# Performance work log

Measured on AMD Instinct MI355X. Metric: run time of the kernel, lower is better.

Reference implementation:

```python
import jax, jax.numpy as jnp
import numpy as np

N_HEAD = 16
ROPE_BASE = 10000.0


def _rope(x):
    # x: (B, T, H, D), interleaved even/odd (GPT-NeoX style)
    B, T, H, D = x.shape
    inv_freq = 1.0 / (ROPE_BASE ** (jnp.arange(0, D, 2, dtype=jnp.float32) / D))
    t = jnp.arange(T, dtype=jnp.float32)
    freqs = t[:, None] * inv_freq[None, :]            # (T, D//2)
    cos = jnp.cos(freqs)[None, :, None, :]            # (1, T, 1, D//2)
    sin = jnp.sin(freqs)[None, :, None, :]
    x1, x2 = x[..., ::2], x[..., 1::2]
    y1 = x1 * cos - x2 * sin
    y2 = x1 * sin + x2 * cos
    return jnp.stack((y1, y2), axis=-1).reshape(B, T, H, D)


def setup_inputs() -> dict:
    key = jax.random.key(0)
    k1, k2, k3 = jax.random.split(key, 3)
    B, T, C = 4, 2048, 1024
    x = jax.random.normal(k1, (B, T, C), dtype=jnp.float32)
    W_attn = jax.random.normal(k2, (C, 3 * C), dtype=jnp.float32) * (1.0 / np.sqrt(C))
    W_proj = jax.random.normal(k3, (C, C), dtype=jnp.float32) * (1.0 / np.sqrt(C))
    return {"x": x, "W_attn": W_attn, "W_proj": W_proj}


def reference(x, W_attn, W_proj):
    B, T, C = x.shape
    H = N_HEAD
    D = C // H
    qkv = jnp.einsum('btc,cf->btf', x, W_attn)        # (B, T, 3C)
    q, k, v = jnp.split(qkv, 3, axis=-1)
    q = _rope(q.reshape(B, T, H, D))
    k = _rope(k.reshape(B, T, H, D))
    v = v.reshape(B, T, H, D)
    # (B, H, T, D)
    q = q.transpose(0, 2, 1, 3)
    k = k.transpose(0, 2, 1, 3)
    v = v.transpose(0, 2, 1, 3)
    scale = 1.0 / np.sqrt(D).astype(np.float32)
    scores = jnp.einsum('bhqd,bhkd->bhqk', q, k) * scale
    causal = jnp.tril(jnp.ones((T, T), dtype=bool))
    scores = jnp.where(causal[None, None], scores, jnp.finfo(scores.dtype).min)
    att = jax.nn.softmax(scores, axis=-1)
    y = jnp.einsum('bhqk,bhkd->bhqd', att, v)         # (B, H, T, D)
    y = y.transpose(0, 2, 1, 3).reshape(B, T, C)
    return jnp.einsum('btc,cf->btf', y, W_proj)
```

## Files before the change

kernel.cpp:

```cpp
#include <hip/hip_runtime.h>
#include <hip/hip_bf16.h>
#include <math.h>

typedef __attribute__((ext_vector_type(8))) __bf16 bf16x8;
typedef __attribute__((ext_vector_type(4))) float f32x4;
typedef __attribute__((ext_vector_type(16))) float f32x16;
typedef __attribute__((ext_vector_type(4))) unsigned short us4;

#define DEVINL static __device__ __forceinline__

DEVINL unsigned short f2bf(float f) {
  union { float f; unsigned int u; } v; v.f = f;
  return (unsigned short)((v.u + 0x7FFFu + ((v.u >> 16) & 1u)) >> 16);
}

DEVINL unsigned short f2bf_hw(float f) {
  __bf16 h = (__bf16)f;
  union { __bf16 h; unsigned short u; } v; v.h = h;
  return v.u;
}

DEVINL unsigned pk2(float a, float b) {
  return (unsigned)f2bf_hw(a) | ((unsigned)f2bf_hw(b) << 16);
}

DEVINL f32x4 mfma16(bf16x8 a, bf16x8 b, f32x4 c) {
  return __builtin_amdgcn_mfma_f32_16x16x32_bf16(a, b, c, 0, 0, 0);
}
DEVINL f32x16 mfma32(bf16x8 a, bf16x8 b, f32x16 c) {
  return __builtin_amdgcn_mfma_f32_32x32x16_bf16(a, b, c, 0, 0, 0);
}

#define GLOAD16(GP, LP)                                                        \
  __builtin_amdgcn_global_load_lds(                                            \
      (const __attribute__((address_space(1))) void*)(GP),                     \
      (__attribute__((address_space(3))) void*)(LP), 16, 0, 0)

static constexpr int kB = 4, kT = 2048, kC = 1024, kH = 16, kD = 64;
static constexpr int kM = kB * kT;

__global__ __launch_bounds__(256) void prep_kernel(
    const float* __restrict__ x, unsigned short* __restrict__ xb,
    const float* __restrict__ Wa, unsigned short* __restrict__ WaT,
    const float* __restrict__ Wp, unsigned short* __restrict__ WpT,
    float* __restrict__ cosT, float* __restrict__ sinT) {
  const int blk = blockIdx.x;
  if (blk < 2048) {
    const int n4 = kM * kC / 4;
    for (int i = blk * 256 + threadIdx.x; i < n4; i += 2048 * 256) {
      float4 v = ((const float4*)x)[i];
      us4 o;
      o[0] = f2bf(v.x); o[1] = f2bf(v.y); o[2] = f2bf(v.z); o[3] = f2bf(v.w);
      ((us4*)xb)[i] = o;
    }
  } else if (blk < 2048 + 3072 + 1024) {
    __shared__ float tile[32][33];
    int t = blk - 2048;
    const float* W; unsigned short* WT; int N, bx, by;
    if (t < 3072) { W = Wa; WT = WaT; N = 3072; bx = t % 96; by = t / 96; }
    else { t -= 3072; W = Wp; WT = WpT; N = 1024; bx = t % 32; by = t / 32; }
    const int n0 = bx * 32, k0 = by * 32;
    const int tx = threadIdx.x & 31, ty = threadIdx.x >> 5;
#pragma unroll
    for (int i = 0; i < 4; ++i)
      tile[ty + i * 8][tx] = W[(size_t)(k0 + ty + i * 8) * N + n0 + tx];
    __syncthreads();
#pragma unroll
    for (int i = 0; i < 4; ++i)
      WT[(size_t)(n0 + ty + i * 8) * 1024 + k0 + tx] = f2bf(tile[tx][ty + i * 8]);
  } else {
    int idx = (blk - 6144) * 256 + threadIdx.x;
    int d2 = idx >> 11, t = idx & 2047;
    double ang = (double)t * pow(10000.0, -(double)d2 / 32.0);
    cosT[idx] = (float)cos(ang);
    sinT[idx] = (float)sin(ang);
  }
}

template <int EPI>
__global__ __launch_bounds__(512, 2) void gemm_bt_kernel(
    const unsigned short* __restrict__ A, const unsigned short* __restrict__ Bt,
    float* __restrict__ Cout, int Ndim, int Kdim,
    const float* __restrict__ cosT, const float* __restrict__ sinT,
    unsigned short* __restrict__ Qr, unsigned short* __restrict__ Kr,
    unsigned short* __restrict__ Vtg) {
  __shared__ unsigned short As[3][256 * 64];
  __shared__ unsigned short Bs[3][128 * 64];
  const int tid = threadIdx.x;
  const int wave = tid >> 6, lane = tid & 63;

  const int nwg = gridDim.x * gridDim.y;
  const int lin = blockIdx.y * gridDim.x + blockIdx.x;
  const int wg = (lin & 7) * (nwg >> 3) + (lin >> 3);
  const int n0 = (wg % gridDim.x) * 128, m0 = (wg / gridDim.x) * 256;

  const int wr = wave >> 1, wc = wave & 1;

  f32x4 acc[4][4] = {};

  const int fr = lane & 15;
  const int sblk = tid;
  const int srow3 = sblk >> 3, skb = sblk & 7;
  const int sgran = (skb ^ (srow3 & 7)) << 3;

  auto stageA = [&](int t, int l) {
    const int bb = t % 3;
    const int k0 = t << 6;
    const int row = (l << 6) + srow3;
    GLOAD16(A + (size_t)(m0 + row) * Kdim + k0 + sgran,
            &As[bb][(l * 512 + wave * 64) * 8]);
  };
  auto stageB = [&](int t, int l) {
    const int bb = t % 3;
    const int k0 = t << 6;
    const int row = (l << 6) + srow3;
    GLOAD16(Bt + (size_t)(n0 + row) * Kdim + k0 + sgran,
            &Bs[bb][(l * 512 + wave * 64) * 8]);
  };

  const int NT = Kdim >> 6;

  stageA(0, 0); stageA(0, 1); stageA(0, 2); stageA(0, 3);
  stageB(0, 0); stageB(0, 1);
  stageA(1, 0); stageA(1, 1); stageA(1, 2); stageA(1, 3);
  stageB(1, 0); stageB(1, 1);
  asm volatile("s_waitcnt vmcnt(6)" ::: "memory");
  __builtin_amdgcn_sched_barrier(0);
  __builtin_amdgcn_s_barrier();

  const int rx = lane & 7, ku = lane >> 4;

  for (int t = 0; t < NT; ++t) {
    const int buf = t % 3;
    const unsigned char* Ab = (const unsigned char*)As[buf];
    const unsigned char* Bb = (const unsigned char*)Bs[buf];
    bf16x8 af[4], bfr[4];

    {
      const int col = ((ku ^ rx) << 4);
#pragma unroll
      for (int f = 0; f < 4; ++f)
        af[f] = *(const bf16x8*)(Ab + (wr * 64 + f * 16 + fr) * 128 + col);
#pragma unroll
      for (int f = 0; f < 4; ++f)
        bfr[f] = *(const bf16x8*)(Bb + (wc * 64 + f * 16 + fr) * 128 + col);
    }
    if (t + 2 < NT) { stageA(t + 2, 0); stageA(t + 2, 1); stageB(t + 2, 0); }
    __builtin_amdgcn_s_barrier();
    asm volatile("s_waitcnt lgkmcnt(0)" ::: "memory");
    __builtin_amdgcn_sched_barrier(0);
    __builtin_amdgcn_s_setprio(1);
#pragma unroll
    for (int i = 0; i < 4; ++i)
#pragma unroll
      for (int j = 0; j < 4; ++j)
        acc[i][j] = mfma16(af[i], bfr[j], acc[i][j]);
    __builtin_amdgcn_s_setprio(0);
    __builtin_amdgcn_s_barrier();

    {
      const int col = (((4 | ku) ^ rx) << 4);
#pragma unroll
      for (int f = 0; f < 4; ++f)
        af[f] = *(const bf16x8*)(Ab + (wr * 64 + f * 16 + fr) * 128 + col);
#pragma unroll
      for (int f = 0; f < 4; ++f)
        bfr[f] = *(const bf16x8*)(Bb + (wc * 64 + f * 16 + fr) * 128 + col);
    }
    if (t + 2 < NT) { stageA(t + 2, 2); stageA(t + 2, 3); stageB(t + 2, 1); }
    if (t + 2 < NT) {
      asm volatile("s_waitcnt vmcnt(6)" ::: "memory");
    } else if (t + 1 < NT) {
      asm volatile("s_waitcnt vmcnt(0)" ::: "memory");
    }
    __builtin_amdgcn_sched_barrier(0);
    __builtin_amdgcn_s_barrier();
    asm volatile("s_waitcnt lgkmcnt(0)" ::: "memory");
    __builtin_amdgcn_sched_barrier(0);
    __builtin_amdgcn_s_setprio(1);
#pragma unroll
    for (int i = 0; i < 4; ++i)
#pragma unroll
      for (int j = 0; j < 4; ++j)
        acc[i][j] = mfma16(af[i], bfr[j], acc[i][j]);
    __builtin_amdgcn_s_setprio(0);
    __builtin_amdgcn_s_barrier();
  }

  const int lr = (lane >> 4) * 4;
  const int fc = lane & 15;
  if (EPI == 0) {
#pragma unroll
    for (int i = 0; i < 4; ++i) {
      int mb = m0 + wr * 64 + i * 16 + lr;
#pragma unroll
      for (int j = 0; j < 4; ++j) {
        int n = n0 + wc * 64 + j * 16 + fc;
#pragma unroll
        for (int r = 0; r < 4; ++r)
          Cout[(size_t)(mb + r) * Ndim + n] = acc[i][j][r];
      }
    }
  } else {
#pragma unroll
    for (int i = 0; i < 4; ++i) {
      int mb = m0 + wr * 64 + i * 16 + lr;
      int b = mb >> 11, t0 = mb & 2047;
#pragma unroll
      for (int j = 0; j < 4; ++j) {
        int n = n0 + wc * 64 + j * 16 + fc;
        int sec = n >> 10;
        int c = n & 1023;
        int h = c >> 6, d = c & 63;
        size_t bh = (size_t)(b * 16 + h);
        if (sec == 2) {
          us4 pk;
#pragma unroll
          for (int r = 0; r < 4; ++r) pk[r] = f2bf(acc[i][j][r]);
          *(us4*)&Vtg[(bh * 64 + d) * 2048 + t0] = pk;
        } else {
          unsigned short* dst = (sec == 0) ? Qr : Kr;
          float4 c4 = *(const float4*)&cosT[(d >> 1) * 2048 + t0];
          float4 s4 = *(const float4*)&sinT[(d >> 1) * 2048 + t0];
          const float* cp = (const float*)&c4;
          const float* sp = (const float*)&s4;
#pragma unroll
          for (int r = 0; r < 4; ++r) {
            float v = acc[i][j][r];
            float pv = __shfl_xor(v, 1);
            float y = (d & 1) ? fmaf(pv, sp[r], v * cp[r])
                              : fmaf(v, cp[r], -pv * sp[r]);
            dst[(bh * 2048 + t0 + r) * 64 + d] = f2bf(y);
          }
        }
      }
    }
  }
}

__global__ __launch_bounds__(256, 3)
void attn_kernel(const unsigned short* __restrict__ Qr,
                 const unsigned short* __restrict__ Kr,
                 const unsigned short* __restrict__ Vtg,
                 unsigned short* __restrict__ Yb) {
  __shared__ unsigned short Ks[3][64 * 64];
  __shared__ unsigned short Vs[3][64 * 64];

  const int tid = threadIdx.x;
  const int wave = tid >> 6, lane = tid & 63;
  const int q31 = lane & 31, hi = lane >> 5;
  const int srow = lane >> 3;
  const int sblk = (lane & 7) ^ srow;
  const int rswz = (lane & 7) << 4;

  int lin = blockIdx.y * 8 + blockIdx.x;
  int wg = (lin & 7) * 64 + (lin >> 3);
  const int qpair = wg & 7;
  const int bh = wg >> 3;

  const unsigned short* Qg = Qr + (size_t)bh * 2048 * 64;
  const unsigned short* Kg = Kr + (size_t)bh * 2048 * 64;
  const unsigned short* Vg = Vtg + (size_t)bh * 64 * 2048;

  const float c = 0.18033688f;
  const float THR = 44.0f;

  auto stage = [&](int j, int bb) {
    int kv0s = j * 64;
#pragma unroll
    for (int o = 0; o < 2; ++o) {
      int s = o * 4 + wave;
      int row = s * 8 + srow;
      GLOAD16(Kg + ((size_t)(kv0s + row) * 64 + sblk * 8), &Ks[bb][s * 512]);
      GLOAD16(Vg + ((size_t)row * 2048 + kv0s + sblk * 8), &Vs[bb][s * 512]);
    }
  };

  for (int seg = 0; seg < 2; ++seg) {
    const int qblk = seg ? (15 - qpair) : qpair;
    const int qw = qblk * 128 + wave * 32;
    const int qg = qw + q31;
    const int NT = 2 * qblk + 2;

    bf16x8 qf[4];
#pragma unroll
    for (int ds = 0; ds < 4; ++ds)
      qf[ds] = *(const bf16x8*)&Qg[(size_t)qg * 64 + ds * 16 + hi * 8];

    float mrow = -1e30f, lrow = 0.f;
    f32x16 y0 = {}, y1 = {};

    stage(0, 0);
    stage(1, 1);
    asm volatile("s_waitcnt vmcnt(4)" ::: "memory");
    __builtin_amdgcn_sched_barrier(0);
    __builtin_amdgcn_s_barrier();

    for (int t = 0; t < NT; ++t) {
      const int buf = t % 3;
      if (t + 2 < NT) stage(t + 2, (t + 2) % 3);
      __builtin_amdgcn_sched_barrier(0);
      const int kv0 = t * 64;

      if (kv0 <= qw + 31) {
        f32x16 st[2] = {};
        __builtin_amdgcn_s_setprio(1);
#pragma unroll
        for (int sub = 0; sub < 2; ++sub) {
          const unsigned char* kbase =
              (const unsigned char*)Ks[buf] + (sub * 32 + q31) * 128;
#pragma unroll
          for (int ds = 0; ds < 4; ++ds) {
            bf16x8 af = *(const bf16x8*)(kbase + ((ds * 32 + hi * 16) ^ rswz));
            st[sub] = mfma32(af, qf[ds], st[sub]);
          }
        }
        __builtin_amdgcn_s_setprio(0);

        if (kv0 + 63 > qw) {
#pragma unroll
          for (int sub = 0; sub < 2; ++sub)
#pragma unroll
            for (int r = 0; r < 16; ++r) {
              int kv = kv0 + sub * 32 + (r & 3) + 8 * (r >> 2) + 4 * hi;
              if (kv > qg) st[sub][r] = -1e30f;
            }
        }

        float tm = st[0][0];
#pragma unroll
        for (int r = 1; r < 16; ++r) tm = fmaxf(tm, st[0][r]);
#pragma unroll
        for (int r = 0; r < 16; ++r) tm = fmaxf(tm, st[1][r]);
        tm = fmaxf(tm, __shfl_xor(tm, 32));

        if (!__all(tm <= mrow + THR)) {
          float mn = fmaxf(mrow, tm);
          float al = __builtin_amdgcn_exp2f((mrow - mn) * c);
          mrow = mn;
          lrow *= al;
#pragma unroll
          for (int r = 0; r < 16; ++r) { y0[r] *= al; y1[r] *= al; }
        }

        const float mc = mrow * c;
        float ps = 0.f;
        unsigned pkw[2][8];
#pragma unroll
        for (int sub = 0; sub < 2; ++sub)
#pragma unroll
          for (int j = 0; j < 8; ++j) {
            float pa = __builtin_amdgcn_exp2f(fmaf(st[sub][2 * j], c, -mc));
            float pb = __builtin_amdgcn_exp2f(fmaf(st[sub][2 * j + 1], c, -mc));
            ps += pa + pb;
            pkw[sub][j] = pk2(pa, pb);
          }
        ps += __shfl_xor(ps, 32);
        lrow += ps;

        __builtin_amdgcn_s_setprio(1);
#pragma unroll
        for (int sub = 0; sub < 2; ++sub) {
#pragma unroll
          for (int ksl = 0; ksl < 2; ++ksl) {
            unsigned w0 = pkw[sub][ksl * 4 + 0], w2 = pkw[sub][ksl * 4 + 2];
            unsigned w1 = pkw[sub][ksl * 4 + 1], w3 = pkw[sub][ksl * 4 + 3];
            asm volatile("v_permlane32_swap_b32 %0, %1" : "+v"(w0), "+v"(w2));
            asm volatile("v_permlane32_swap_b32 %0, %1" : "+v"(w1), "+v"(w3));
            union { bf16x8 v; unsigned u[4]; } pf;
            pf.u[0] = w0; pf.u[1] = w1; pf.u[2] = w2; pf.u[3] = w3;
            const int cb = sub * 64 + ksl * 32 + hi * 16;
#pragma unroll
            for (int dm = 0; dm < 2; ++dm) {
              const int row = dm * 32 + q31;
              bf16x8 vf = *(const bf16x8*)((const unsigned char*)Vs[buf] +
                                           row * 128 + (cb ^ rswz));
              if (dm == 0) y0 = mfma32(vf, pf.v, y0);
              else         y1 = mfma32(vf, pf.v, y1);
            }
          }
        }
        __builtin_amdgcn_s_setprio(0);
      }

      asm volatile("s_waitcnt lgkmcnt(0)" ::: "memory");
      __builtin_amdgcn_sched_barrier(0);
      if (t + 2 < NT) {
        asm volatile("s_waitcnt vmcnt(4)" ::: "memory");
      } else if (t + 1 < NT) {
        asm volatile("s_waitcnt vmcnt(0)" ::: "memory");
      }
      __builtin_amdgcn_sched_barrier(0);
      __builtin_amdgcn_s_barrier();
    }

    const int b = bh >> 4, h = bh & 15;
    float inv = __builtin_amdgcn_rcpf(lrow);
    unsigned short* yrow = Yb + (size_t)(b * 2048 + qg) * 1024 + h * 64;
#pragma unroll
    for (int dm = 0; dm < 2; ++dm)
#pragma unroll
      for (int g = 0; g < 4; ++g) {
        us4 o;
#pragma unroll
        for (int e = 0; e < 4; ++e) {
          float yv = dm ? y1[g * 4 + e] : y0[g * 4 + e];
          o[e] = f2bf_hw(yv * inv);
        }
        *(us4*)&yrow[dm * 32 + g * 8 + hi * 4] = o;
      }
  }
}

extern "C" void kernel_launch(void* const* d_in, const int* in_sizes, int n_in,
                              void* d_out, int out_size, void* d_ws,
                              size_t ws_size, hipStream_t stream) {
  const float* x = (const float*)d_in[0];
  const float* Wa = (const float*)d_in[1];
  const float* Wp = (const float*)d_in[2];
  float* out = (float*)d_out;
  char* ws = (char*)d_ws;

  constexpr size_t OFF_WAT = 0;
  constexpr size_t OFF_WPT = 6291456;
  constexpr size_t OFF_COS = 8388608;
  constexpr size_t OFF_SIN = 8650752;
  constexpr size_t OFF_XB  = 8912896;
  constexpr size_t OFF_Q   = 25690112;
  constexpr size_t OFF_K   = 42467328;
  constexpr size_t OFF_V   = 59244544;

  unsigned short* WaT = (unsigned short*)(ws + OFF_WAT);
  unsigned short* WpT = (unsigned short*)(ws + OFF_WPT);
  float* cosT = (float*)(ws + OFF_COS);
  float* sinT = (float*)(ws + OFF_SIN);
  unsigned short* xb = (unsigned short*)(ws + OFF_XB);
  unsigned short* Yb = xb;
  unsigned short* Qr = (unsigned short*)(ws + OFF_Q);
  unsigned short* Kr = (unsigned short*)(ws + OFF_K);
  unsigned short* Vt = (unsigned short*)(ws + OFF_V);

  prep_kernel<<<2048 + 3072 + 1024 + 256, 256, 0, stream>>>(
      x, xb, Wa, WaT, Wp, WpT, cosT, sinT);

  gemm_bt_kernel<1><<<dim3(24, 32), 512, 0, stream>>>(
      xb, WaT, nullptr, 3072, 1024, cosT, sinT, Qr, Kr, Vt);

  attn_kernel<<<dim3(8, 64), 256, 0, stream>>>(Qr, Kr, Vt, Yb);

  gemm_bt_kernel<0><<<dim3(8, 32), 512, 0, stream>>>(
      Yb, WpT, out, 1024, 1024, nullptr, nullptr, nullptr, nullptr, nullptr);
}
```

Before: 177.0 us.

## Defer PV MFMAs to next iteration to overlap with QK and softmax

Software-pipelines the attention inner loop. The P·V matrix multiplies for tile t are held back and issued in iteration t+1, after that iteration's QK^T MFMAs, so they can overlap with the softmax exp work. To make this work, the V fragments are read from LDS into registers and the permuted P words are kept in registers. A drain step after the loop issues the last pending PV. The row-max is also rewritten as a tree reduction to shorten the dependency chain. The extra live registers (V fragments plus P words) raise VGPR pressure and may reduce occupancy or cause spills.

```diff
diff --git a/kernel.cpp b/kernel.cpp
--- a/kernel.cpp
+++ b/kernel.cpp
@@ -290,6 +290,10 @@
     float mrow = -1e30f, lrow = 0.f;
     f32x16 y0 = {}, y1 = {};
 
+    unsigned pfw[4][4];
+    bf16x8 vreg[8];
+    bool pend = false;
+
     stage(0, 0);
     stage(1, 1);
     asm volatile("s_waitcnt vmcnt(4)" ::: "memory");
@@ -301,9 +305,10 @@
       if (t + 2 < NT) stage(t + 2, (t + 2) % 3);
       __builtin_amdgcn_sched_barrier(0);
       const int kv0 = t * 64;
-
-      if (kv0 <= qw + 31) {
-        f32x16 st[2] = {};
+      const bool active = (kv0 <= qw + 31);
+
+      f32x16 st[2] = {};
+      if (active) {
         __builtin_amdgcn_s_setprio(1);
 #pragma unroll
         for (int sub = 0; sub < 2; ++sub) {
@@ -316,7 +321,23 @@
           }
         }
         __builtin_amdgcn_s_setprio(0);
-
+      }
+
+      if (pend) {
+        __builtin_amdgcn_s_setprio(1);
+#pragma unroll
+        for (int g = 0; g < 4; ++g) {
+          union { bf16x8 v; unsigned u[4]; } pf;
+          pf.u[0] = pfw[g][0]; pf.u[1] = pfw[g][1];
+          pf.u[2] = pfw[g][2]; pf.u[3] = pfw[g][3];
+          y0 = mfma32(vreg[g * 2 + 0], pf.v, y0);
+          y1 = mfma32(vreg[g * 2 + 1], pf.v, y1);
+        }
+        __builtin_amdgcn_s_setprio(0);
+        pend = false;
+      }
+
+      if (active) {
         if (kv0 + 63 > qw) {
 #pragma unroll
           for (int sub = 0; sub < 2; ++sub)
@@ -327,12 +348,14 @@
             }
         }
 
-        float tm = st[0][0];
-#pragma unroll
-        for (int r = 1; r < 16; ++r) tm = fmaxf(tm, st[0][r]);
-#pragma unroll
-        for (int r = 0; r < 16; ++r) tm = fmaxf(tm, st[1][r]);
-        tm = fmaxf(tm, __shfl_xor(tm, 32));
+        float m[16];
+#pragma unroll
+        for (int r = 0; r < 16; ++r) m[r] = fmaxf(st[0][r], st[1][r]);
+#pragma unroll
+        for (int s = 8; s >= 1; s >>= 1)
+#pragma unroll
+          for (int r = 0; r < s; ++r) m[r] = fmaxf(m[r], m[r + s]);
+        float tm = fmaxf(m[0], __shfl_xor(m[0], 32));
 
         if (!__all(tm <= mrow + THR)) {
           float mn = fmaxf(mrow, tm);
@@ -345,42 +368,43 @@
 
         const float mc = mrow * c;
         float ps = 0.f;
-        unsigned pkw[2][8];
-#pragma unroll
-        for (int sub = 0; sub < 2; ++sub)
+#pragma unroll
+        for (int sub = 0; sub < 2; ++sub) {
+          unsigned pw[8];
 #pragma unroll
           for (int j = 0; j < 8; ++j) {
             float pa = __builtin_amdgcn_exp2f(fmaf(st[sub][2 * j], c, -mc));
             float pb = __builtin_amdgcn_exp2f(fmaf(st[sub][2 * j + 1], c, -mc));
             ps += pa + pb;
-            pkw[sub][j] = pk2(pa, pb);
+            pw[j] = pk2(pa, pb);
           }
+#pragma unroll
+          for (int ksl = 0; ksl < 2; ++ksl) {
+            unsigned w0 = pw[ksl * 4 + 0], w2 = pw[ksl * 4 + 2];
+            unsigned w1 = pw[ksl * 4 + 1], w3 = pw[ksl * 4 + 3];
+            asm volatile("v_permlane32_swap_b32 %0, %1" : "+v"(w0), "+v"(w2));
+            asm volatile("v_permlane32_swap_b32 %0, %1" : "+v"(w1), "+v"(w3));
+            pfw[sub * 2 + ksl][0] = w0; pfw[sub * 2 + ksl][1] = w1;
+            pfw[sub * 2 + ksl][2] = w2; pfw[sub * 2 + ksl][3] = w3;
+          }
+        }
         ps += __shfl_xor(ps, 32);
         lrow += ps;
 
-        __builtin_amdgcn_s_setprio(1);
-#pragma unroll
-        for (int sub = 0; sub < 2; ++sub) {
+#pragma unroll
+        for (int sub = 0; sub < 2; ++sub)
 #pragma unroll
           for (int ksl = 0; ksl < 2; ++ksl) {
-            unsigned w0 = pkw[sub][ksl * 4 + 0], w2 = pkw[sub][ksl * 4 + 2];
-            unsigned w1 = pkw[sub][ksl * 4 + 1], w3 = pkw[sub][ksl * 4 + 3];
-            asm volatile("v_permlane32_swap_b32 %0, %1" : "+v"(w0), "+v"(w2));
-            asm volatile("v_permlane32_swap_b32 %0, %1" : "+v"(w1), "+v"(w3));
-            union { bf16x8 v; unsigned u[4]; } pf;
-            pf.u[0] = w0; pf.u[1] = w1; pf.u[2] = w2; pf.u[3] = w3;
             const int cb = sub * 64 + ksl * 32 + hi * 16;
 #pragma unroll
             for (int dm = 0; dm < 2; ++dm) {
               const int row = dm * 32 + q31;
-              bf16x8 vf = *(const bf16x8*)((const unsigned char*)Vs[buf] +
-                                           row * 128 + (cb ^ rswz));
-              if (dm == 0) y0 = mfma32(vf, pf.v, y0);
-              else         y1 = mfma32(vf, pf.v, y1);
+              vreg[(sub * 2 + ksl) * 2 + dm] =
+                  *(const bf16x8*)((const unsigned char*)Vs[buf] + row * 128 +
+                                   (cb ^ rswz));
             }
           }
-        }
-        __builtin_amdgcn_s_setprio(0);
+        pend = true;
       }
 
       asm volatile("s_waitcnt lgkmcnt(0)" ::: "memory");
@@ -392,6 +416,17 @@
       }
       __builtin_amdgcn_sched_barrier(0);
       __builtin_amdgcn_s_barrier();
+    }
+
+    if (pend) {
+#pragma unroll
+      for (int g = 0; g < 4; ++g) {
+        union { bf16x8 v; unsigned u[4]; } pf;
+        pf.u[0] = pfw[g][0]; pf.u[1] = pfw[g][1];
+        pf.u[2] = pfw[g][2]; pf.u[3] = pfw[g][3];
+        y0 = mfma32(vreg[g * 2 + 0], pf.v, y0);
+        y1 = mfma32(vreg[g * 2 + 1], pf.v, y1);
+      }
     }
 
     const int b = bh >> 4, h = bh & 15;
```

Result: slower. 197.8 us (+11.8%).
